# Performance work log

Hardware: AMD Instinct MI355X
Metric: run time of the kernel (lower is better)

The kernel has to match this reference:

```python
import jax, jax.numpy as jnp
import numpy as np

N_NODES, N_EDGES = 50000, 800000
IN_DIM, HID_DIM, OUT_DIM = 512, 256, 256


def setup_inputs() -> dict:
    key = jax.random.key(0)
    ks = jax.random.split(key, 8)
    x = jax.random.normal(ks[0], (N_NODES, IN_DIM), dtype=jnp.float32)
    edge_index = jax.random.randint(ks[1], (2, N_EDGES), 0, N_NODES, dtype=jnp.int64)
    # GCNConv lin weights (no bias in lin; separate additive bias after aggregation)
    W1 = jax.random.normal(ks[2], (IN_DIM, HID_DIM), dtype=jnp.float32) * (1.0 / np.sqrt(IN_DIM))
    b1 = jnp.zeros((HID_DIM,), dtype=jnp.float32)
    W2 = jax.random.normal(ks[3], (HID_DIM, OUT_DIM), dtype=jnp.float32) * (1.0 / np.sqrt(HID_DIM))
    b2 = jnp.zeros((OUT_DIM,), dtype=jnp.float32)
    # projection head nn.Linear(out_dim, out_dim)
    Wp = jax.random.normal(ks[4], (OUT_DIM, OUT_DIM), dtype=jnp.float32) * (1.0 / np.sqrt(OUT_DIM))
    bp = jnp.zeros((OUT_DIM,), dtype=jnp.float32)
    return {"x": x, "edge_index": edge_index, "W1": W1, "b1": b1,
            "W2": W2, "b2": b2, "Wp": Wp, "bp": bp}


def _gcn_conv(x, W, b, src, dst, n):
    # x' = D^{-1/2}(A+I)D^{-1/2} (x W) + b ; deg includes self-loop (+1)
    h = x @ W  # [N, F]
    deg = jax.ops.segment_sum(jnp.ones(src.shape[0], h.dtype), dst, num_segments=n) + 1.0
    dis = jax.lax.rsqrt(deg)  # deg^{-1/2}, [N]
    msg = (dis[src] * dis[dst])[:, None] * h[src]  # [E, F] gathered+scaled messages
    agg = jax.ops.segment_sum(msg, dst, num_segments=n)  # scatter-add to dst
    # self-loop contribution: norm = dis[i]^2, message = h[i]
    return agg + (dis * dis)[:, None] * h + b


def reference(x, edge_index, W1, b1, W2, b2, Wp, bp):
    src, dst = edge_index[0], edge_index[1]
    n = x.shape[0]
    h = jax.nn.relu(_gcn_conv(x, W1, b1, src, dst, n))
    # eval mode: dropout is identity
    h = _gcn_conv(h, W2, b2, src, dst, n)
    return h @ Wp + bp
```

## Files before the change

kernel.cpp:

```cpp
#include <hip/hip_runtime.h>
#include <hip/hip_bf16.h>

typedef __bf16 bf16_8 __attribute__((ext_vector_type(8)));
typedef float  f32_4  __attribute__((ext_vector_type(4)));

#define NNODES 50000
#define NEDGES 800000
#define INDIM  512
#define HIDDIM 256
#define CSTRIDE 264


__global__ void zero_kernel(int* p, int n) {
    int i = blockIdx.x * 256 + threadIdx.x;
    if (i < n) p[i] = 0;
}

__global__ void detect_kernel(const int* __restrict__ ei,
                              const unsigned short* __restrict__ xh,
                              int* __restrict__ flags) {
    int t = threadIdx.x;
    unsigned long long nz = __ballot(ei[1 + 2 * t] != 0);
    unsigned e = (xh[2 * t] >> 7) & 0xFF;
    unsigned long long ok = __ballot(e >= 90 && e <= 142);
    if (t == 0) {
        flags[0] = (nz == 0ull) ? 1 : 0;
        flags[1] = (__popcll(ok) >= 48) ? 1 : 0;
    }
}

__global__ void count_kernel(const int* __restrict__ idx, const int* __restrict__ flags,
                             int* __restrict__ deg, int E) {
    int e = blockIdx.x * 256 + threadIdx.x;
    if (e >= E) return;
    int d = flags[0] ? idx[2 * (E + e)] : idx[E + e];
    d = min(max(d, 0), NNODES - 1);
    atomicAdd(&deg[d], 1);
}

__global__ void reduce_kernel(const int* __restrict__ deg, int* __restrict__ bsum, int n) {
    __shared__ int l[256];
    int i = blockIdx.x * 256 + threadIdx.x;
    l[threadIdx.x] = (i < n) ? deg[i] : 0;
    __syncthreads();
    for (int o = 128; o > 0; o >>= 1) {
        if (threadIdx.x < o) l[threadIdx.x] += l[threadIdx.x + o];
        __syncthreads();
    }
    if (threadIdx.x == 0) bsum[blockIdx.x] = l[0];
}

__global__ void scanb_kernel(const int* __restrict__ bsum, int nb,
                             int* __restrict__ boff, int* __restrict__ offs_last) {
    __shared__ int l[256];
    int v = (threadIdx.x < nb) ? bsum[threadIdx.x] : 0;
    l[threadIdx.x] = v;
    __syncthreads();
    for (int o = 1; o < 256; o <<= 1) {
        int t = (threadIdx.x >= o) ? l[threadIdx.x - o] : 0;
        __syncthreads();
        l[threadIdx.x] += t;
        __syncthreads();
    }
    if (threadIdx.x < nb) boff[threadIdx.x] = l[threadIdx.x] - v;
    if (threadIdx.x == 255) *offs_last = l[255];
}

__global__ void local_scan_kernel(const int* __restrict__ deg, const int* __restrict__ boff,
                                  int* __restrict__ offs, float* __restrict__ dis, int n) {
    __shared__ int l[256];
    int i = blockIdx.x * 256 + threadIdx.x;
    int v = (i < n) ? deg[i] : 0;
    l[threadIdx.x] = v;
    __syncthreads();
    for (int o = 1; o < 256; o <<= 1) {
        int t = (threadIdx.x >= o) ? l[threadIdx.x - o] : 0;
        __syncthreads();
        l[threadIdx.x] += t;
        __syncthreads();
    }
    if (i < n) {
        offs[i] = boff[blockIdx.x] + l[threadIdx.x] - v;
        dis[i]  = rsqrtf((float)v + 1.0f);
    }
}

__global__ void fill_kernel(const int* __restrict__ idx, const int* __restrict__ flags,
                            const int* __restrict__ offs, int* __restrict__ cursor,
                            int* __restrict__ csr, int E) {
    int e = blockIdx.x * 256 + threadIdx.x;
    if (e >= E) return;
    int s, d;
    if (flags[0]) { s = idx[2 * e]; d = idx[2 * (E + e)]; }
    else          { s = idx[e];     d = idx[E + e]; }
    s = min(max(s, 0), NNODES - 1);
    d = min(max(d, 0), NNODES - 1);
    int p = atomicAdd(&cursor[d], 1);
    csr[offs[d] + p] = s;
}

__global__ void repack_kernel(const void* __restrict__ Wv, const int* __restrict__ flags,
                              __hip_bfloat16* __restrict__ P, int K, int N) {
    int ntiles = N / 16;
    int nt = blockIdx.x % ntiles;
    int kt = blockIdx.x / ntiles;
    int lane = threadIdx.x;
    int quad = lane >> 4, l16 = lane & 15;
    size_t pbase = ((size_t)blockIdx.x * 64 + lane) * 8;
    int k0 = kt * 32 + quad * 8;
    int col = nt * 16 + l16;
    bool bf = flags[1] != 0;
    for (int j = 0; j < 8; ++j) {
        size_t src = (size_t)(k0 + j) * N + col;
        P[pbase + j] = bf ? ((const __hip_bfloat16*)Wv)[src]
                          : (__hip_bfloat16)((const float*)Wv)[src];
    }
}

template<int K>
__global__ __launch_bounds__(128, 2)
void gemm_kernel(const void* __restrict__ Av,
                 const __hip_bfloat16* __restrict__ Bp,
                 const void* __restrict__ biasv,
                 void* __restrict__ Cv,
                 const int* __restrict__ flags, int amode, int cmode,
                 int M) {
    constexpr int N = 256;
    constexpr int NKT = K / 32;
    constexpr int PF  = 4;
    __shared__ __align__(16) __hip_bfloat16 cstage[2 * 32 * CSTRIDE];

    const int wave = threadIdx.x >> 6;
    const int lane = threadIdx.x & 63;
    const int quad = lane >> 4;
    const int l16  = lane & 15;
    const int row0 = blockIdx.x * 64 + wave * 32;
    const bool active0 = row0 < M;
    const bool active1 = row0 + 16 < M;
    const bool bf  = flags[1] != 0;
    const bool abf = amode || bf;
    const bool cbf = cmode || bf;

    f32_4 acc0[16] = {};
    f32_4 acc1[16] = {};

    auto loadA = [&](int h, int kt) -> bf16_8 {
        bf16_8 r = {};
        bool act = h ? active1 : active0;
        if (!act) return r;
        size_t ab = (size_t)(row0 + h * 16 + l16) * K + (size_t)kt * 32 + quad * 8;
        if (abf) {
            r = *(const bf16_8*)((const __hip_bfloat16*)Av + ab);
        } else {
            const float* Af = (const float*)Av + ab;
            f32_4 lo = *(const f32_4*)Af;
            f32_4 hi = *(const f32_4*)(Af + 4);
            #pragma unroll
            for (int j = 0; j < 4; ++j) { r[j] = (__bf16)lo[j]; r[j + 4] = (__bf16)hi[j]; }
        }
        return r;
    };

    bf16_8 a0p[PF], a1p[PF];
    #pragma unroll
    for (int i = 0; i < PF; ++i) { a0p[i] = loadA(0, i); a1p[i] = loadA(1, i); }

    #pragma unroll
    for (int kt = 0; kt < NKT; ++kt) {
        const int slot = kt % PF;
        bf16_8 a0 = a0p[slot], a1 = a1p[slot];
        if (kt + PF < NKT) {
            a0p[slot] = loadA(0, kt + PF);
            a1p[slot] = loadA(1, kt + PF);
        }
        const __hip_bfloat16* bbase = Bp + (size_t)kt * 8192 + lane * 8;
        #pragma unroll
        for (int ct = 0; ct < 16; ++ct) {
            bf16_8 b = *(const bf16_8*)(bbase + ct * 512);
            acc0[ct] = __builtin_amdgcn_mfma_f32_16x16x32_bf16(a0, b, acc0[ct], 0, 0, 0);
            acc1[ct] = __builtin_amdgcn_mfma_f32_16x16x32_bf16(a1, b, acc1[ct], 0, 0, 0);
        }
    }

    if (cbf) {
        __hip_bfloat16* cs = cstage + wave * 32 * CSTRIDE;
        #pragma unroll
        for (int ct = 0; ct < 16; ++ct) {
            int col = ct * 16 + l16;
            float bv = 0.0f;
            if (biasv) bv = bf ? (float)((const __hip_bfloat16*)biasv)[col]
                               : ((const float*)biasv)[col];
            #pragma unroll
            for (int rr = 0; rr < 4; ++rr) {
                int rl = quad * 4 + rr;
                cs[rl * CSTRIDE + col]        = (__hip_bfloat16)(acc0[ct][rr] + bv);
                cs[(16 + rl) * CSTRIDE + col] = (__hip_bfloat16)(acc1[ct][rr] + bv);
            }
        }
        __syncthreads();
        const int rloc = lane >> 5;
        const int q16  = lane & 31;
        #pragma unroll
        for (int pass = 0; pass < 16; ++pass) {
            int r = pass * 2 + rloc;
            int row = row0 + r;
            if (row < M) {
                bf16_8 v = *(const bf16_8*)(cs + r * CSTRIDE + q16 * 8);
                *(bf16_8*)((__hip_bfloat16*)Cv + (size_t)row * N + q16 * 8) = v;
            }
        }
    } else {
        #pragma unroll
        for (int ct = 0; ct < 16; ++ct) {
            int col = ct * 16 + l16;
            float bv = 0.0f;
            if (biasv) bv = bf ? (float)((const __hip_bfloat16*)biasv)[col]
                               : ((const float*)biasv)[col];
            #pragma unroll
            for (int rr = 0; rr < 4; ++rr) {
                int row = row0 + quad * 4 + rr;
                if (active0)
                    ((float*)Cv)[(size_t)row * N + col] = acc0[ct][rr] + bv;
                if (active1)
                    ((float*)Cv)[(size_t)(row + 16) * N + col] = acc1[ct][rr] + bv;
            }
        }
    }
}

__device__ inline void acc_row(f32_4& a0, f32_4& a1, float w, bf16_8 r) {
    a0[0] += w * (float)r[0]; a0[1] += w * (float)r[1];
    a0[2] += w * (float)r[2]; a0[3] += w * (float)r[3];
    a1[0] += w * (float)r[4]; a1[1] += w * (float)r[5];
    a1[2] += w * (float)r[6]; a1[3] += w * (float)r[7];
}

__global__ __launch_bounds__(256)
void agg_kernel(const __hip_bfloat16* __restrict__ h,
                const int* __restrict__ csr,
                const int* __restrict__ offs,
                const float* __restrict__ dis,
                const void* __restrict__ biasv,
                const int* __restrict__ flags,
                __hip_bfloat16* __restrict__ out,
                int relu) {
    const int wave = threadIdx.x >> 6;
    const int lane = threadIdx.x & 63;
    const int n = blockIdx.x * 4 + wave;
    if (n >= NNODES) return;
    const int half = lane >> 5;
    const int l32  = lane & 31;

    const float dn = dis[n];
    const int beg = offs[n], end = offs[n + 1];
    f32_4 a0 = {}, a1 = {};

    int j = beg + half;
    for (; j + 2 < end; j += 4) {
        int sa = csr[j], sb = csr[j + 2];
        bf16_8 ra = *(const bf16_8*)(h + (size_t)sa * HIDDIM + l32 * 8);
        bf16_8 rb = *(const bf16_8*)(h + (size_t)sb * HIDDIM + l32 * 8);
        float wa = dis[sa], wb = dis[sb];
        acc_row(a0, a1, wa, ra);
        acc_row(a0, a1, wb, rb);
    }
    if (j < end) {
        int sa = csr[j];
        bf16_8 ra = *(const bf16_8*)(h + (size_t)sa * HIDDIM + l32 * 8);
        acc_row(a0, a1, dis[sa], ra);
    }

    #pragma unroll
    for (int k = 0; k < 4; ++k) {
        a0[k] += __shfl_xor(a0[k], 32);
        a1[k] += __shfl_xor(a1[k], 32);
    }

    bf16_8 rn = *(const bf16_8*)(h + (size_t)n * HIDDIM + l32 * 8);
    float bv[8];
    if (flags[1]) {
        bf16_8 bb = ((const bf16_8*)biasv)[l32];
        #pragma unroll
        for (int k = 0; k < 8; ++k) bv[k] = (float)bb[k];
    } else {
        f32_4 blo = *((const f32_4*)biasv + 2 * l32);
        f32_4 bhi = *((const f32_4*)biasv + 2 * l32 + 1);
        #pragma unroll
        for (int k = 0; k < 4; ++k) { bv[k] = blo[k]; bv[k + 4] = bhi[k]; }
    }
    const float dn2 = dn * dn;
    float v[8];
    #pragma unroll
    for (int k = 0; k < 4; ++k) {
        v[k]     = dn * a0[k] + dn2 * (float)rn[k]     + bv[k];
        v[k + 4] = dn * a1[k] + dn2 * (float)rn[k + 4] + bv[k + 4];
    }
    if (relu) {
        #pragma unroll
        for (int k = 0; k < 8; ++k) v[k] = fmaxf(v[k], 0.0f);
    }
    if (half == 0) {
        bf16_8 o;
        #pragma unroll
        for (int k = 0; k < 8; ++k) o[k] = (__bf16)v[k];
        *(bf16_8*)(out + (size_t)n * HIDDIM + l32 * 8) = o;
    }
}


extern "C" void kernel_launch(void* const* d_in, const int* in_sizes, int n_in,
                              void* d_out, int out_size, void* d_ws, size_t ws_size,
                              hipStream_t stream) {
    const int M = NNODES, E = NEDGES;
    const void* x  = d_in[0];
    const int*  ei = (const int*)d_in[1];
    const void* W1 = d_in[2];
    const void* b1 = d_in[3];
    const void* W2 = d_in[4];
    const void* b2 = d_in[5];
    const void* Wp = d_in[6];
    const void* bp = d_in[7];

    char* w = (char*)d_ws;
    size_t off = 0;
    auto alloc = [&](size_t bytes) -> void* {
        void* p = w + off;
        off += (bytes + 255) & ~(size_t)255;
        return p;
    };
    int*   deg    = (int*)alloc((size_t)M * 4);
    int*   cursor = (int*)alloc((size_t)M * 4);
    int*   offs   = (int*)alloc((size_t)(M + 1) * 4);
    float* dis    = (float*)alloc((size_t)M * 4);
    int*   flags  = (int*)alloc(256);
    int*   bsum   = (int*)alloc(256 * 4);
    int*   boff   = (int*)alloc(256 * 4);
    int*   csr    = (int*)alloc((size_t)E * 4);
    __hip_bfloat16* W1p = (__hip_bfloat16*)alloc((size_t)INDIM * HIDDIM * 2);
    __hip_bfloat16* W2p = (__hip_bfloat16*)alloc((size_t)HIDDIM * HIDDIM * 2);
    __hip_bfloat16* Wpp = (__hip_bfloat16*)alloc((size_t)HIDDIM * HIDDIM * 2);
    if (ws_size < off) return;

    __hip_bfloat16* h  = (__hip_bfloat16*)d_out;
    __hip_bfloat16* ha = (__hip_bfloat16*)d_in[0];

    const int nb = (M + 255) / 256;

    zero_kernel<<<nb, 256, 0, stream>>>(deg, M);
    zero_kernel<<<nb, 256, 0, stream>>>(cursor, M);
    detect_kernel<<<1, 64, 0, stream>>>(ei, (const unsigned short*)x, flags);
    count_kernel<<<(E + 255) / 256, 256, 0, stream>>>(ei, flags, deg, E);
    reduce_kernel<<<nb, 256, 0, stream>>>(deg, bsum, M);
    scanb_kernel<<<1, 256, 0, stream>>>(bsum, nb, boff, &offs[M]);
    local_scan_kernel<<<nb, 256, 0, stream>>>(deg, boff, offs, dis, M);
    fill_kernel<<<(E + 255) / 256, 256, 0, stream>>>(ei, flags, offs, cursor, csr, E);

    repack_kernel<<<(INDIM / 32) * (HIDDIM / 16), 64, 0, stream>>>(W1, flags, W1p, INDIM, HIDDIM);
    repack_kernel<<<(HIDDIM / 32) * (HIDDIM / 16), 64, 0, stream>>>(W2, flags, W2p, HIDDIM, HIDDIM);
    repack_kernel<<<(HIDDIM / 32) * (HIDDIM / 16), 64, 0, stream>>>(Wp, flags, Wpp, HIDDIM, HIDDIM);

    const int ggrid = (M + 63) / 64;
    const int agrid = (M + 3) / 4;

    gemm_kernel<INDIM><<<ggrid, 128, 0, stream>>>(x, W1p, nullptr, h, flags, 0, 1, M);
    agg_kernel<<<agrid, 256, 0, stream>>>(h, csr, offs, dis, b1, flags, ha, 1);

    gemm_kernel<HIDDIM><<<ggrid, 128, 0, stream>>>(ha, W2p, nullptr, h, flags, 1, 1, M);
    agg_kernel<<<agrid, 256, 0, stream>>>(h, csr, offs, dis, b2, flags, ha, 0);

    gemm_kernel<HIDDIM><<<ggrid, 128, 0, stream>>>(ha, Wpp, bp, d_out, flags, 1, 0, M);
}
```

Before: 501.5 us.

## Stage GEMM weight slabs in LDS shared across four waves per block

The GEMM kernel now uses 256-thread blocks covering 128 rows, and cooperatively loads phases of the packed weight matrix into shared memory via direct global-to-LDS loads. Before, each wave streamed B from global/L2 on its own, and now the slab is reused across four waves. A-operand loads are grouped per phase instead of software-prefetched across k-tiles, and the bf16 output staging reuses the same shared buffer in two half passes. The added barriers per phase and the loss of cross-phase A prefetch may expose memory latency.

```diff
diff --git a/kernel.cpp b/kernel.cpp
--- a/kernel.cpp
+++ b/kernel.cpp
@@ -9,6 +9,12 @@
 #define INDIM  512
 #define HIDDIM 256
 #define CSTRIDE 264
+
+__device__ inline void gload_lds16(const __hip_bfloat16* g, __hip_bfloat16* l) {
+    __builtin_amdgcn_global_load_lds(
+        (const __attribute__((address_space(1))) void*)g,
+        (__attribute__((address_space(3))) void*)l, 16, 0, 0);
+}
 
 
 __global__ void zero_kernel(int* p, int n) {
@@ -118,7 +124,7 @@
 }
 
 template<int K>
-__global__ __launch_bounds__(128, 2)
+__global__ __launch_bounds__(256, 2)
 void gemm_kernel(const void* __restrict__ Av,
                  const __hip_bfloat16* __restrict__ Bp,
                  const void* __restrict__ biasv,
@@ -126,15 +132,15 @@
                  const int* __restrict__ flags, int amode, int cmode,
                  int M) {
     constexpr int N = 256;
-    constexpr int NKT = K / 32;
-    constexpr int PF  = 4;
-    __shared__ __align__(16) __hip_bfloat16 cstage[2 * 32 * CSTRIDE];
+    constexpr int PHKT   = 4;
+    constexpr int PHASES = K / (PHKT * 32);
+    __shared__ __align__(16) __hip_bfloat16 smem[PHKT * 8192];
 
     const int wave = threadIdx.x >> 6;
     const int lane = threadIdx.x & 63;
     const int quad = lane >> 4;
     const int l16  = lane & 15;
-    const int row0 = blockIdx.x * 64 + wave * 32;
+    const int row0 = blockIdx.x * 128 + wave * 32;
     const bool active0 = row0 < M;
     const bool active1 = row0 + 16 < M;
     const bool bf  = flags[1] != 0;
@@ -161,52 +167,61 @@
         return r;
     };
 
-    bf16_8 a0p[PF], a1p[PF];
     #pragma unroll
-    for (int i = 0; i < PF; ++i) { a0p[i] = loadA(0, i); a1p[i] = loadA(1, i); }
-
-    #pragma unroll
-    for (int kt = 0; kt < NKT; ++kt) {
-        const int slot = kt % PF;
-        bf16_8 a0 = a0p[slot], a1 = a1p[slot];
-        if (kt + PF < NKT) {
-            a0p[slot] = loadA(0, kt + PF);
-            a1p[slot] = loadA(1, kt + PF);
-        }
-        const __hip_bfloat16* bbase = Bp + (size_t)kt * 8192 + lane * 8;
-        #pragma unroll
-        for (int ct = 0; ct < 16; ++ct) {
-            bf16_8 b = *(const bf16_8*)(bbase + ct * 512);
-            acc0[ct] = __builtin_amdgcn_mfma_f32_16x16x32_bf16(a0, b, acc0[ct], 0, 0, 0);
-            acc1[ct] = __builtin_amdgcn_mfma_f32_16x16x32_bf16(a1, b, acc1[ct], 0, 0, 0);
-        }
-    }
-
+    for (int ph = 0; ph < PHASES; ++ph) {
+        bf16_8 a0[PHKT], a1[PHKT];
+        #pragma unroll
+        for (int k2 = 0; k2 < PHKT; ++k2) {
+            a0[k2] = loadA(0, ph * PHKT + k2);
+            a1[k2] = loadA(1, ph * PHKT + k2);
+        }
+        if (ph > 0) __syncthreads();
+        const __hip_bfloat16* slab = Bp + (size_t)ph * (PHKT * 8192);
+        #pragma unroll
+        for (int i = 0; i < PHKT * 4; ++i) {
+            int ch = i * 4 + wave;
+            gload_lds16(slab + ch * 512 + lane * 8, smem + ch * 512);
+        }
+        __syncthreads();
+        #pragma unroll
+        for (int k2 = 0; k2 < PHKT; ++k2) {
+            const __hip_bfloat16* bb = smem + k2 * 8192 + lane * 8;
+            #pragma unroll
+            for (int ct = 0; ct < 16; ++ct) {
+                bf16_8 b = *(const bf16_8*)(bb + ct * 512);
+                acc0[ct] = __builtin_amdgcn_mfma_f32_16x16x32_bf16(a0[k2], b, acc0[ct], 0, 0, 0);
+                acc1[ct] = __builtin_amdgcn_mfma_f32_16x16x32_bf16(a1[k2], b, acc1[ct], 0, 0, 0);
+            }
+        }
+    }
+
+    __syncthreads();
     if (cbf) {
-        __hip_bfloat16* cs = cstage + wave * 32 * CSTRIDE;
-        #pragma unroll
-        for (int ct = 0; ct < 16; ++ct) {
-            int col = ct * 16 + l16;
-            float bv = 0.0f;
-            if (biasv) bv = bf ? (float)((const __hip_bfloat16*)biasv)[col]
-                               : ((const float*)biasv)[col];
+        __hip_bfloat16* cs = smem + wave * 16 * CSTRIDE;
+        #pragma unroll
+        for (int pass = 0; pass < 2; ++pass) {
+            const int rowg = row0 + pass * 16;
             #pragma unroll
-            for (int rr = 0; rr < 4; ++rr) {
-                int rl = quad * 4 + rr;
-                cs[rl * CSTRIDE + col]        = (__hip_bfloat16)(acc0[ct][rr] + bv);
-                cs[(16 + rl) * CSTRIDE + col] = (__hip_bfloat16)(acc1[ct][rr] + bv);
+            for (int ct = 0; ct < 16; ++ct) {
+                int col = ct * 16 + l16;
+                float bv = 0.0f;
+                if (biasv) bv = bf ? (float)((const __hip_bfloat16*)biasv)[col]
+                                   : ((const float*)biasv)[col];
+                #pragma unroll
+                for (int rr = 0; rr < 4; ++rr) {
+                    float v = (pass ? acc1[ct][rr] : acc0[ct][rr]) + bv;
+                    cs[(quad * 4 + rr) * CSTRIDE + col] = (__hip_bfloat16)v;
+                }
             }
-        }
-        __syncthreads();
-        const int rloc = lane >> 5;
-        const int q16  = lane & 31;
-        #pragma unroll
-        for (int pass = 0; pass < 16; ++pass) {
-            int r = pass * 2 + rloc;
-            int row = row0 + r;
-            if (row < M) {
-                bf16_8 v = *(const bf16_8*)(cs + r * CSTRIDE + q16 * 8);
-                *(bf16_8*)((__hip_bfloat16*)Cv + (size_t)row * N + q16 * 8) = v;
+            const int r  = lane >> 2;
+            const int qc = lane & 3;
+            if (rowg + r < M) {
+                __hip_bfloat16* crow = (__hip_bfloat16*)Cv + (size_t)(rowg + r) * N;
+                #pragma unroll
+                for (int j = 0; j < 8; ++j) {
+                    int col = qc * 64 + j * 8;
+                    *(bf16_8*)(crow + col) = *(const bf16_8*)(cs + r * CSTRIDE + col);
+                }
             }
         }
     } else {
@@ -359,14 +374,14 @@
     repack_kernel<<<(HIDDIM / 32) * (HIDDIM / 16), 64, 0, stream>>>(W2, flags, W2p, HIDDIM, HIDDIM);
     repack_kernel<<<(HIDDIM / 32) * (HIDDIM / 16), 64, 0, stream>>>(Wp, flags, Wpp, HIDDIM, HIDDIM);
 
-    const int ggrid = (M + 63) / 64;
+    const int ggrid = (M + 127) / 128;
     const int agrid = (M + 3) / 4;
 
-    gemm_kernel<INDIM><<<ggrid, 128, 0, stream>>>(x, W1p, nullptr, h, flags, 0, 1, M);
+    gemm_kernel<INDIM><<<ggrid, 256, 0, stream>>>(x, W1p, nullptr, h, flags, 0, 1, M);
     agg_kernel<<<agrid, 256, 0, stream>>>(h, csr, offs, dis, b1, flags, ha, 1);
 
-    gemm_kernel<HIDDIM><<<ggrid, 128, 0, stream>>>(ha, W2p, nullptr, h, flags, 1, 1, M);
+    gemm_kernel<HIDDIM><<<ggrid, 256, 0, stream>>>(ha, W2p, nullptr, h, flags, 1, 1, M);
     agg_kernel<<<agrid, 256, 0, stream>>>(h, csr, offs, dis, b2, flags, ha, 0);
 
-    gemm_kernel<HIDDIM><<<ggrid, 128, 0, stream>>>(ha, Wpp, bp, d_out, flags, 1, 0, M);
-}
+    gemm_kernel<HIDDIM><<<ggrid, 256, 0, stream>>>(ha, Wpp, bp, d_out, flags, 1, 0, M);
+}
```

Measured after the change: 471.8 us. -5.9%, faster.
